# Kernel tuning notes

Measured on AMD Instinct MI355X. Metric: run time of the kernel, lower is better.

## Reference

```python
import jax, jax.numpy as jnp
import numpy as np

L, D, H, DK, S, B = 6, 1024, 16, 64, 512, 8
DFF = 4 * D
NEG = -1.0e9


def layer_norm(x, g, b, eps=1e-5):
    mu = jnp.mean(x, axis=-1, keepdims=True)
    var = jnp.var(x, axis=-1, keepdims=True)
    return (x - mu) * jax.lax.rsqrt(var + eps) * g + b


def setup_inputs() -> dict:
    key = jax.random.key(0)
    ks = jax.random.split(key, 16)
    s = 0.02
    inp = {
        "x": jax.random.normal(ks[0], (B, S, D), jnp.float32),
        "mask": jax.random.bernoulli(ks[1], 0.1, (B, S, S)),
        "relation": jax.random.normal(ks[2], (B, S, S), jnp.float32) * 0.1,
        # per-layer params (stacked over L)
        "Wq": jax.random.normal(ks[3], (L, D, H * DK), jnp.float32) * s,
        "Wk": jax.random.normal(ks[4], (L, D, H * DK), jnp.float32) * s,
        "Wv": jax.random.normal(ks[5], (L, D, H * DK), jnp.float32) * s,
        "Wo": jax.random.normal(ks[6], (L, H * DK, D), jnp.float32) * s,
        "bo": jnp.zeros((L, D), jnp.float32),
        "ln_g": jnp.ones((L, D), jnp.float32),   # EncoderLayer.norm (shared pre-attn / pre-FFN)
        "ln_b": jnp.zeros((L, D), jnp.float32),
        "ln2_g": jnp.ones((L, D), jnp.float32),  # AttSubLayerv2.norm
        "ln2_b": jnp.zeros((L, D), jnp.float32),
        "W1": jax.random.normal(ks[7], (L, D, DFF), jnp.float32) * s,
        "b1": jnp.zeros((L, DFF), jnp.float32),
        "W2": jax.random.normal(ks[8], (L, DFF, D), jnp.float32) * s,
        "b2": jnp.zeros((L, D), jnp.float32),
        "lnf_g": jnp.ones((D,), jnp.float32),    # Encoder.norm
        "lnf_b": jnp.zeros((D,), jnp.float32),
    }
    return inp


def reference(x, mask, relation, Wq, Wk, Wv, Wo, bo, ln_g, ln_b, ln2_g, ln2_b,
              W1, b1, W2, b2, lnf_g, lnf_b):
    # dropout layers run in eval mode (identity)
    scale = 1.0 / jnp.sqrt(jnp.asarray(DK, x.dtype))
    h = x
    attns = []
    for l in range(L):
        q_in = layer_norm(h, ln_g[l], ln_b[l])
        # AttSubLayerv2
        def proj(W):
            return jnp.einsum('bsd,de->bse', q_in, W).reshape(h.shape[0], -1, H, DK).transpose(0, 2, 1, 3)
        Q, K, V = proj(Wq[l]), proj(Wk[l]), proj(Wv[l])  # [B,H,S,DK]
        qk = jnp.einsum('bhqd,bhkd->bhqk', Q, K)
        scores = jnp.einsum('bhqk,bkn->bhqn', qk, relation) * scale
        scores = jnp.where(mask[:, None], NEG, scores)
        p = jax.nn.softmax(scores, axis=-1)  # [B,H,S,S]
        att = jnp.einsum('bhqk,bhkd->bhqd', p, V).transpose(0, 2, 1, 3).reshape(h.shape[0], -1, H * DK)
        att = att @ Wo[l] + bo[l]
        att_out = layer_norm(att + q_in, ln2_g[l], ln2_b[l])
        h = h + att_out
        # FFN (pre-norm with shared EncoderLayer norm)
        f = layer_norm(h, ln_g[l], ln_b[l])
        h = h + (jax.nn.relu(f @ W1[l] + b1[l]) @ W2[l] + b2[l])
        attns.append(p)
    out = layer_norm(h, lnf_g, lnf_b)
    return out, jnp.stack(attns)
```

## Files before the change

### kernel.cpp

```cpp
#include <hip/hip_runtime.h>
#include <hip/hip_bf16.h>
#include <stdint.h>

#define LL 6
#define DD 1024
#define HH 16
#define DKK 64
#define SS 512
#define BB 8
#define DFF_ 4096
#define BS (BB*SS)
#define NEGV -1.0e9f

typedef __attribute__((ext_vector_type(8))) short short8;
typedef __attribute__((ext_vector_type(4))) float f32x4;
typedef __attribute__((ext_vector_type(4))) unsigned short ushort4v;

static __device__ __forceinline__ float bf2f(unsigned short u){
  union { unsigned int i; float f; } v; v.i = ((unsigned int)u)<<16; return v.f;
}
static __device__ __forceinline__ unsigned short f2bf(float f){
  union { float f; unsigned int i; } v; v.f=f;
  unsigned int r = v.i + 0x7fff + ((v.i>>16)&1);
  return (unsigned short)(r>>16);
}

static __device__ __forceinline__ void gload16(const void* g, void* l){
  __builtin_amdgcn_global_load_lds((const __attribute__((address_space(1))) unsigned int*)g,
                                   (__attribute__((address_space(3))) unsigned int*)l, 16, 0, 0);
}

struct TrDesc { const float* in; unsigned short* out; long is1,is2,os1,os2; int ldin,ldout,zd,gx,gy; };
struct TrPack { TrDesc d[7]; int cum[8]; };

__global__ void __launch_bounds__(256) tr_multi_k(TrPack P)
{
  __shared__ float t[32][33];
  int bid=blockIdx.x, di=0;
  #pragma unroll
  for(int k=1;k<7;k++) if(bid>=P.cum[k]) di=k;
  TrDesc dd=P.d[di];
  int local=bid-P.cum[di];
  int bx=local%dd.gx; int rest=local/dd.gx;
  int by=rest%dd.gy; int z=rest/dd.gy;
  int z1=z/dd.zd, z2=z%dd.zd;
  const float* ip=dd.in+z1*dd.is1+z2*dd.is2;
  unsigned short* op=dd.out+z1*dd.os1+z2*dd.os2;
  int r0=by*32, c0=bx*32;
  int tx=threadIdx.x, ty=threadIdx.y;
  #pragma unroll
  for(int i=0;i<4;i++)
    t[ty+i*8][tx] = ip[(long)(r0+ty+i*8)*dd.ldin + c0+tx];
  __syncthreads();
  #pragma unroll
  for(int i=0;i<4;i++)
    op[(long)(c0+ty+i*8)*dd.ldout + r0+tx] = f2bf(t[tx][ty+i*8]);
}

__global__ void __launch_bounds__(256) maskpack_k(const int* __restrict__ mask, unsigned* __restrict__ mb)
{
  int idx = blockIdx.x*256 + threadIdx.x;
  int row = idx>>4, w = idx&15;
  const int* mp = mask + (long)row*SS + w*32;
  unsigned v=0;
  #pragma unroll
  for(int i=0;i<32;i++) v |= (mp[i]!=0) ? (1u<<i) : 0u;
  mb[idx]=v;
}

__global__ void __launch_bounds__(256) ln_k(const float* __restrict__ src,
    const float* __restrict__ gw, const float* __restrict__ bw,
    float* __restrict__ outf, unsigned short* __restrict__ outb,
    const float* __restrict__ resid)
{
  long row=blockIdx.x;
  float4 v=((const float4*)(src+row*DD))[threadIdx.x];
  float s=v.x+v.y+v.z+v.w;
  float s2=v.x*v.x+v.y*v.y+v.z*v.z+v.w*v.w;
  #pragma unroll
  for(int o=32;o;o>>=1){ s+=__shfl_xor(s,o); s2+=__shfl_xor(s2,o); }
  __shared__ float red[8];
  int wid=threadIdx.x>>6, lane=threadIdx.x&63;
  if(lane==0){ red[wid]=s; red[4+wid]=s2; }
  __syncthreads();
  s=red[0]+red[1]+red[2]+red[3];
  s2=red[4]+red[5]+red[6]+red[7];
  float mu=s*(1.f/DD);
  float rstd=rsqrtf(s2*(1.f/DD)-mu*mu+1e-5f);
  int c=threadIdx.x*4;
  float4 g4=*(const float4*)(gw+c), b4=*(const float4*)(bw+c);
  float4 o;
  o.x=(v.x-mu)*rstd*g4.x+b4.x;
  o.y=(v.y-mu)*rstd*g4.y+b4.y;
  o.z=(v.z-mu)*rstd*g4.z+b4.z;
  o.w=(v.w-mu)*rstd*g4.w+b4.w;
  if(resid){
    float4 r4=((const float4*)(resid+row*DD))[threadIdx.x];
    o.x+=r4.x; o.y+=r4.y; o.z+=r4.z; o.w+=r4.w;
  }
  if(outf) ((float4*)(outf+row*DD))[threadIdx.x]=o;
  if(outb){
    uint2 pk;
    pk.x=(unsigned)f2bf(o.x)|((unsigned)f2bf(o.y)<<16);
    pk.y=(unsigned)f2bf(o.z)|((unsigned)f2bf(o.w)<<16);
    ((uint2*)(outb+row*DD))[threadIdx.x]=pk;
  }
}

__global__ void __launch_bounds__(256) ln2_k(const float* __restrict__ src,
    const float* __restrict__ resid,
    const float* __restrict__ g2, const float* __restrict__ b2,
    const float* __restrict__ g1, const float* __restrict__ b1,
    float* __restrict__ outf, unsigned short* __restrict__ outb)
{
  long row=blockIdx.x;
  int wid=threadIdx.x>>6, lane=threadIdx.x&63, c=threadIdx.x*4;
  __shared__ float red[8];
  float4 v=((const float4*)(src+row*DD))[threadIdx.x];
  float s=v.x+v.y+v.z+v.w;
  float s2=v.x*v.x+v.y*v.y+v.z*v.z+v.w*v.w;
  #pragma unroll
  for(int o=32;o;o>>=1){ s+=__shfl_xor(s,o); s2+=__shfl_xor(s2,o); }
  if(lane==0){ red[wid]=s; red[4+wid]=s2; }
  __syncthreads();
  s=red[0]+red[1]+red[2]+red[3];
  s2=red[4]+red[5]+red[6]+red[7];
  float mu=s*(1.f/DD);
  float rstd=rsqrtf(s2*(1.f/DD)-mu*mu+1e-5f);
  float4 g4=*(const float4*)(g2+c), b4=*(const float4*)(b2+c);
  float4 r4=((const float4*)(resid+row*DD))[threadIdx.x];
  float4 o;
  o.x=(v.x-mu)*rstd*g4.x+b4.x+r4.x;
  o.y=(v.y-mu)*rstd*g4.y+b4.y+r4.y;
  o.z=(v.z-mu)*rstd*g4.z+b4.z+r4.z;
  o.w=(v.w-mu)*rstd*g4.w+b4.w+r4.w;
  ((float4*)(outf+row*DD))[threadIdx.x]=o;
  s=o.x+o.y+o.z+o.w;
  s2=o.x*o.x+o.y*o.y+o.z*o.z+o.w*o.w;
  #pragma unroll
  for(int of=32;of;of>>=1){ s+=__shfl_xor(s,of); s2+=__shfl_xor(s2,of); }
  __syncthreads();
  if(lane==0){ red[wid]=s; red[4+wid]=s2; }
  __syncthreads();
  s=red[0]+red[1]+red[2]+red[3];
  s2=red[4]+red[5]+red[6]+red[7];
  mu=s*(1.f/DD);
  rstd=rsqrtf(s2*(1.f/DD)-mu*mu+1e-5f);
  g4=*(const float4*)(g1+c); b4=*(const float4*)(b1+c);
  uint2 pk;
  pk.x=(unsigned)f2bf((o.x-mu)*rstd*g4.x+b4.x)|((unsigned)f2bf((o.y-mu)*rstd*g4.y+b4.y)<<16);
  pk.y=(unsigned)f2bf((o.z-mu)*rstd*g4.z+b4.z)|((unsigned)f2bf((o.w-mu)*rstd*g4.w+b4.w)<<16);
  ((uint2*)(outb+row*DD))[threadIdx.x]=pk;
}

struct GemmP {
  const unsigned short* A; long sA1; int ldA;
  const unsigned short* B; long sB1; int ldB;
  float* outF; unsigned short* outB; long sO1; int ldO;
  const float* bias;
  const float* residF; int ldR;
  const unsigned short* residB;
  unsigned short *kt, *vt;
  int K, relu, mb;
};

template<int MODE,int BM,int BN,int WM,int WN>
__global__ void __launch_bounds__(WM*WN*64,2) gemm2p_k(GemmP p)
{
  constexpr int NW=WM*WN, BK=64;
  constexpr int WRT=BM/WM, WCT=BN/WN;
  constexpr int FM=WRT/16, FN=WCT/16;
  constexpr int RG=NW*8;
  constexpr int BUFE=(BM+BN)*BK;
  __shared__ __align__(16) unsigned short smem[2*BUFE];
  const int tid=threadIdx.x, lane=tid&63, wid=tid>>6;
  const int wr=wid/WN, wc=wid%WN;
  const int lr=lane&15, lk=(lane>>4)*8;
  const int nwg=gridDim.x, bid=blockIdx.x;
  const int nb=(bid&7)*(nwg>>3)+(bid>>3);
  const int m0=(nb%p.mb)*BM, n0=(nb/p.mb)*BN;
  const int z=blockIdx.y;
  const unsigned short* Ap=p.A+(long)z*p.sA1;
  const unsigned short* Bp=p.B+(long)z*p.sB1;
  const int NT=p.K/BK;

  const int sr8=lane>>3;
  const int scol=((lane&7)^sr8)<<3;

  #define STG(T,BI) { \
    const long kb_=(long)(T)*BK; \
    unsigned short* As_=smem+(BI)*BUFE; \
    unsigned short* Bs_=As_+BM*BK; \
    _Pragma("unroll") \
    for(int L=0;L<BM/RG;L++){ int r_=L*RG+wid*8+sr8; \
      gload16(Ap+(long)(m0+r_)*p.ldA+kb_+scol, As_+(L*RG+wid*8)*BK); } \
    _Pragma("unroll") \
    for(int L=0;L<BN/RG;L++){ int r_=L*RG+wid*8+sr8; \
      gload16(Bp+(long)(n0+r_)*p.ldB+kb_+scol, Bs_+(L*RG+wid*8)*BK); } }

  f32x4 acc[FM][FN];
  #pragma unroll
  for(int m=0;m<FM;m++)
    #pragma unroll
    for(int n=0;n<FN;n++) acc[m][n]=(f32x4){0.f,0.f,0.f,0.f};

  STG(0,0);
  asm volatile("s_waitcnt vmcnt(0)" ::: "memory");
  __builtin_amdgcn_sched_barrier(0);
  __builtin_amdgcn_s_barrier();
  __builtin_amdgcn_sched_barrier(0);

  const int xr=(lr&7)<<3;
  int cur=0;
  for(int t=0;t<NT;t++){
    if(t+1<NT) STG(t+1,cur^1);
    const unsigned short* As=smem+cur*BUFE;
    const unsigned short* Bs=As+BM*BK;
    #pragma unroll
    for(int kk=0;kk<2;kk++){
      short8 a[FM], b[FN];
      #pragma unroll
      for(int m=0;m<FM;m++) a[m]=*(const short8*)(As+(wr*WRT+m*16+lr)*BK+((kk*32+lk)^xr));
      #pragma unroll
      for(int n=0;n<FN;n++) b[n]=*(const short8*)(Bs+(wc*WCT+n*16+lr)*BK+((kk*32+lk)^xr));
      __builtin_amdgcn_s_setprio(1);
      #pragma unroll
      for(int m=0;m<FM;m++)
        #pragma unroll
        for(int n=0;n<FN;n++)
          acc[m][n]=__builtin_amdgcn_mfma_f32_16x16x32_bf16(a[m],b[n],acc[m][n],0,0,0);
      __builtin_amdgcn_s_setprio(0);
    }
    asm volatile("s_waitcnt vmcnt(0)" ::: "memory");
    __builtin_amdgcn_sched_barrier(0);
    __builtin_amdgcn_s_barrier();
    __builtin_amdgcn_sched_barrier(0);
    cur^=1;
  }
  #undef STG

  const int rl=(lane>>4)*4;
  if(MODE==1){
    int sec = n0>>10;
    #pragma unroll
    for(int m=0;m<FM;m++){
      int gr0 = m0 + wr*WRT + m*16 + rl;
      int b = gr0>>9, s0 = gr0&511;
      #pragma unroll
      for(int n=0;n<FN;n++){
        int gc = n0 + wc*WCT + n*16 + lr;
        if(sec==0){
          #pragma unroll
          for(int r=0;r<4;r++)
            p.outB[(long)(gr0+r)*1024 + gc] = f2bf(acc[m][n][r]);
        } else {
          unsigned short* dst = sec==1 ? p.kt : p.vt;
          int hh=(gc>>6)&15, d=gc&63;
          ushort4v pk;
          pk.x=f2bf(acc[m][n][0]); pk.y=f2bf(acc[m][n][1]);
          pk.z=f2bf(acc[m][n][2]); pk.w=f2bf(acc[m][n][3]);
          *(ushort4v*)(dst + (((long)b*HH+hh)*DKK+d)*SS + s0) = pk;
        }
      }
    }
  } else {
    #pragma unroll
    for(int m=0;m<FM;m++){
      int gr0 = m0 + wr*WRT + m*16 + rl;
      #pragma unroll
      for(int n=0;n<FN;n++){
        int gc = n0 + wc*WCT + n*16 + lr;
        float bv = p.bias ? p.bias[gc] : 0.f;
        #pragma unroll
        for(int r=0;r<4;r++){
          long ro=(long)(gr0+r);
          float val=acc[m][n][r]+bv;
          if(p.relu) val=fmaxf(val,0.f);
          if(p.residF) val += p.residF[ro*(long)p.ldR+gc];
          if(p.residB) val += bf2f(p.residB[ro*(long)p.ldR+gc]);
          long oo = (long)z*p.sO1 + ro*(long)p.ldO+gc;
          if(p.outF) p.outF[oo]=val;
          if(p.outB) p.outB[oo]=f2bf(val);
        }
      }
    }
  }
}

template<int MODE,int BM,int BN,int WM,int WN>
static inline void launch_gemm2p(GemmP& p,int M,int N,int Z,hipStream_t s){
  p.mb=M/BM;
  gemm2p_k<MODE,BM,BN,WM,WN><<<dim3((M/BM)*(N/BN),Z),dim3(WM*WN*64),0,s>>>(p);
}

__global__ void __launch_bounds__(512) att_k(const unsigned short* __restrict__ Qb,
    const unsigned short* __restrict__ KRT, float* __restrict__ pout,
    const unsigned* __restrict__ maskb, const unsigned short* __restrict__ Vt,
    unsigned short* __restrict__ attb)
{
  constexpr int BM=128, BK=32, NT=512;
  constexpr int FM=4, FN=8;
  __shared__ __align__(16) char smem[49152];
  unsigned short* As = (unsigned short*)smem;
  unsigned short* Bs = (unsigned short*)(smem+8192);
  unsigned short* Ps = (unsigned short*)smem;
  unsigned short* Vs = (unsigned short*)(smem+32768);
  __shared__ float redmx[BM][4];
  __shared__ float redsm[BM][4];
  int bh = blockIdx.y; int b = bh>>4, h = bh&15;
  const unsigned short* Ap = Qb + (long)b*SS*1024 + h*64;
  const unsigned short* Bp = KRT + (long)b*SS*1024 + h*64;
  int m0 = blockIdx.x*BM;
  int tid=threadIdx.x, lane=tid&63, wid=tid>>6;
  int wr=wid>>2, wc=wid&3;
  f32x4 acc[FM][FN];
  #pragma unroll
  for(int i=0;i<FM;i++)
    #pragma unroll
    for(int j=0;j<FN;j++) acc[i][j]=(f32x4){0.f,0.f,0.f,0.f};
  const int lr=lane&15, lk=(lane>>4)*8;
  for(int k0=0;k0<DKK;k0+=BK){
    { int v=tid;
      gload16(Ap + (long)(m0+(v>>2))*1024 + k0 + (v&3)*8, As + (wid*64)*8); }
    #pragma unroll
    for(int r=0;r<4;r++){
      int v=r*NT+tid;
      gload16(Bp + (long)(v>>2)*1024 + k0 + (v&3)*8, Bs + (r*NT+wid*64)*8);
    }
    __syncthreads();
    short8 af[FM], bfr[FN];
    #pragma unroll
    for(int i=0;i<FM;i++) af[i]=*(const short8*)(As + (wr*64+i*16+lr)*BK + lk);
    #pragma unroll
    for(int j=0;j<FN;j++) bfr[j]=*(const short8*)(Bs + (wc*128+j*16+lr)*BK + lk);
    #pragma unroll
    for(int i=0;i<FM;i++)
      #pragma unroll
      for(int j=0;j<FN;j++)
        acc[i][j]=__builtin_amdgcn_mfma_f32_16x16x32_bf16(af[i],bfr[j],acc[i][j],0,0,0);
    __syncthreads();
  }
  const int rl=(lane>>4)*4;
  #pragma unroll
  for(int i=0;i<FM;i++){
    #pragma unroll
    for(int r=0;r<4;r++){
      int row=wr*64+i*16+rl+r;
      uint4 mw = *((const uint4*)(maskb + ((long)(b*SS+m0+row))*16 + wc*4));
      float m_=-3.4e38f;
      #pragma unroll
      for(int j=0;j<FN;j++){
        unsigned word = (j>>1)==0? mw.x : (j>>1)==1? mw.y : (j>>1)==2? mw.z : mw.w;
        float v = ((word>>(((j&1)<<4)+lr))&1) ? NEGV : acc[i][j][r]*0.125f;
        acc[i][j][r]=v; m_=fmaxf(m_,v);
      }
      #pragma unroll
      for(int o=1;o<16;o<<=1) m_=fmaxf(m_,__shfl_xor(m_,o));
      if(lr==0) redmx[row][wc]=m_;
    }
  }
  __syncthreads();
  #pragma unroll
  for(int i=0;i<FM;i++){
    #pragma unroll
    for(int r=0;r<4;r++){
      int row=wr*64+i*16+rl+r;
      float m_=fmaxf(fmaxf(redmx[row][0],redmx[row][1]),fmaxf(redmx[row][2],redmx[row][3]));
      float s_=0.f;
      #pragma unroll
      for(int j=0;j<FN;j++){
        float e=__expf(acc[i][j][r]-m_);
        acc[i][j][r]=e; s_+=e;
      }
      #pragma unroll
      for(int o=1;o<16;o<<=1) s_+=__shfl_xor(s_,o);
      if(lr==0) redsm[row][wc]=s_;
    }
  }
  __syncthreads();
  #pragma unroll
  for(int i=0;i<FM;i++){
    #pragma unroll
    for(int r=0;r<4;r++){
      int row=wr*64+i*16+rl+r;
      float inv=1.f/(redsm[row][0]+redsm[row][1]+redsm[row][2]+redsm[row][3]);
      long obase=((long)bh*SS + m0+row)*(long)SS;
      #pragma unroll
      for(int j=0;j<FN;j++){
        int col=wc*128+j*16+lr;
        float pv=acc[i][j][r]*inv;
        acc[i][j][r]=pv;
        pout[obase+col]=pv;
      }
    }
  }
  __syncthreads();
  f32x4 attacc[4];
  #pragma unroll
  for(int j=0;j<4;j++) attacc[j]=(f32x4){0.f,0.f,0.f,0.f};
  for(int kc=0;kc<4;kc++){
    #pragma unroll
    for(int r2=0;r2<2;r2++){
      int v=r2*512+tid;
      int d=v>>4, m=v&15;
      int u=m^(d&7);
      gload16(Vt + ((long)bh*64 + d)*512 + kc*128 + u*8, Vs + (r2*512 + wid*64)*8);
    }
    if(wc==kc){
      #pragma unroll
      for(int i=0;i<FM;i++){
        #pragma unroll
        for(int r=0;r<4;r++){
          int row=wr*64+i*16+rl+r;
          #pragma unroll
          for(int j=0;j<FN;j++){
            int col=j*16+lr;
            Ps[row*128 + (col ^ ((row&7)<<3))] = f2bf(acc[i][j][r]);
          }
        }
      }
    }
    __syncthreads();
    #pragma unroll
    for(int kk=0;kk<4;kk++){
      int arow=wid*16+lr;
      short8 paf=*(const short8*)(Ps + arow*128 + ((kk*32+lk) ^ ((arow&7)<<3)));
      #pragma unroll
      for(int j=0;j<4;j++){
        int d=j*16+lr;
        short8 vbf=*(const short8*)(Vs + d*128 + ((kk*32+lk) ^ ((d&7)<<3)));
        attacc[j]=__builtin_amdgcn_mfma_f32_16x16x32_bf16(paf,vbf,attacc[j],0,0,0);
      }
    }
    __syncthreads();
  }
  #pragma unroll
  for(int j=0;j<4;j++){
    #pragma unroll
    for(int r=0;r<4;r++){
      int row = m0 + wid*16 + rl + r;
      attb[((long)b*SS + row)*DD + h*64 + j*16 + lr] = f2bf(attacc[j][r]);
    }
  }
}

extern "C" void kernel_launch(void* const* d_in, const int* in_sizes, int n_in,
                              void* d_out, int out_size, void* d_ws, size_t ws_size,
                              hipStream_t stream)
{
  const float* x    =(const float*)d_in[0];
  const int*   mask =(const int*)d_in[1];
  const float* rel  =(const float*)d_in[2];
  const float* Wq   =(const float*)d_in[3];
  const float* Wk   =(const float*)d_in[4];
  const float* Wv   =(const float*)d_in[5];
  const float* Wo   =(const float*)d_in[6];
  const float* bo   =(const float*)d_in[7];
  const float* ln_g =(const float*)d_in[8];
  const float* ln_b =(const float*)d_in[9];
  const float* ln2_g=(const float*)d_in[10];
  const float* ln2_b=(const float*)d_in[11];
  const float* W1   =(const float*)d_in[12];
  const float* b1   =(const float*)d_in[13];
  const float* W2   =(const float*)d_in[14];
  const float* b2   =(const float*)d_in[15];
  const float* lnf_g=(const float*)d_in[16];
  const float* lnf_b=(const float*)d_in[17];
  float* out=(float*)d_out;

  char* w=(char*)d_ws;
  auto alloc=[&](long bytes)->void*{ void* p=(void*)w; w += (bytes+255)&~255L; return p; };
  unsigned short* WTqkv=(unsigned short*)alloc((long)LL*3072*1024*2);
  unsigned short* WoT  =(unsigned short*)alloc((long)LL*1024*1024*2);
  unsigned short* W1T  =(unsigned short*)alloc((long)LL*DFF_*DD*2);
  unsigned short* W2T  =(unsigned short*)alloc((long)LL*DD*DFF_*2);
  unsigned short* relT =(unsigned short*)alloc((long)BB*SS*SS*2);
  unsigned short* qin_b=(unsigned short*)alloc((long)BS*DD*2);
  unsigned short* Qb   =(unsigned short*)alloc((long)BS*1024*2);
  unsigned short* Vt   =(unsigned short*)alloc((long)BB*HH*DKK*SS*2);
  unsigned short* Kt   =(unsigned short*)alloc((long)BB*HH*DKK*SS*2);
  unsigned short* KRT  =(unsigned short*)alloc((long)BB*SS*1024*2);
  unsigned short* attb =(unsigned short*)alloc((long)BS*DD*2);
  float*          attres=(float*)alloc((long)BS*DD*4);
  unsigned short* gbuf =(unsigned short*)alloc((long)BS*DFF_*2);
  float*          hbuf =(float*)alloc((long)BS*DD*4);
  unsigned*       maskb=(unsigned*)alloc((long)BS*16*4);
  (void)ws_size; (void)in_sizes; (void)n_in; (void)out_size;

  TrPack tp;
  auto set=[&](int i, const float* in, unsigned short* o, int ldin, int ldout,
               long is1, long os1, int zd, long is2, long os2, int gx, int gy){
    tp.d[i]={in,o,is1,is2,os1,os2,ldin,ldout,zd,gx,gy};
  };
  set(0, Wq, WTqkv,           1024,1024,(long)1024*1024,(long)3072*1024,1,0,0, 32,32);
  set(1, Wk, WTqkv+1024*1024, 1024,1024,(long)1024*1024,(long)3072*1024,1,0,0, 32,32);
  set(2, Wv, WTqkv+2048*1024, 1024,1024,(long)1024*1024,(long)3072*1024,1,0,0, 32,32);
  set(3, Wo, WoT,             1024,1024,(long)1024*1024,(long)1024*1024,1,0,0, 32,32);
  set(4, W1, W1T, 4096,1024,(long)1024*4096,(long)1024*4096,1,0,0, 128,32);
  set(5, W2, W2T, 1024,4096,(long)4096*1024,(long)4096*1024,1,0,0, 32,128);
  set(6, rel, relT, 512,512,(long)512*512,(long)512*512,1,0,0, 16,16);
  int nb[7]={32*32*LL,32*32*LL,32*32*LL,32*32*LL,128*32*LL,32*128*LL,16*16*BB};
  tp.cum[0]=0;
  for(int i=0;i<7;i++) tp.cum[i+1]=tp.cum[i]+nb[i];
  tr_multi_k<<<dim3(tp.cum[7]),dim3(32,8),0,stream>>>(tp);
  maskpack_k<<<dim3(BS*16/256),dim3(256),0,stream>>>(mask, maskb);

  const float* hin = x;
  for(int l=0;l<LL;l++){
    ln_k<<<dim3(BS),dim3(256),0,stream>>>(hin, ln_g+l*DD, ln_b+l*DD, (float*)nullptr, qin_b, (const float*)nullptr);
    { GemmP p{}; p.A=qin_b; p.ldA=DD; p.B=WTqkv+(long)l*3072*1024; p.ldB=DD;
      p.outB=Qb; p.kt=Kt; p.vt=Vt; p.K=DD;
      launch_gemm2p<1,256,256,2,4>(p, BS, 3072, 1, stream); }
    { GemmP p{}; p.A=relT; p.sA1=(long)SS*SS; p.ldA=SS;
      p.B=Kt; p.sB1=(long)HH*DKK*SS; p.ldB=SS;
      p.outB=KRT; p.sO1=(long)SS*1024; p.ldO=1024; p.K=SS;
      launch_gemm2p<0,128,128,2,2>(p, SS, 1024, BB, stream); }
    float* attn_l = out + (long)BS*DD + (long)l*BB*HH*SS*SS;
    att_k<<<dim3(SS/128, BB*HH),dim3(512),0,stream>>>(Qb, KRT, attn_l, maskb, Vt, attb);
    { GemmP p{}; p.A=attb; p.ldA=DD; p.B=WoT+(long)l*1024*1024; p.ldB=DD;
      p.outF=attres; p.ldO=DD; p.bias=bo+l*DD;
      p.residB=qin_b; p.ldR=DD; p.K=DD;
      launch_gemm2p<0,128,128,2,2>(p, BS, DD, 1, stream); }
    ln2_k<<<dim3(BS),dim3(256),0,stream>>>(attres, hin, ln2_g+l*DD, ln2_b+l*DD,
        ln_g+l*DD, ln_b+l*DD, hbuf, qin_b);
    { GemmP p{}; p.A=qin_b; p.ldA=DD; p.B=W1T+(long)l*DFF_*DD; p.ldB=DD;
      p.outB=gbuf; p.ldO=DFF_; p.bias=b1+l*DFF_; p.relu=1; p.K=DD;
      launch_gemm2p<0,256,256,2,4>(p, BS, DFF_, 1, stream); }
    { GemmP p{}; p.A=gbuf; p.ldA=DFF_; p.B=W2T+(long)l*DD*DFF_; p.ldB=DFF_;
      p.outF=hbuf; p.ldO=DD; p.bias=b2+l*DD;
      p.residF=hbuf; p.ldR=DD; p.K=DFF_;
      launch_gemm2p<0,128,128,2,2>(p, BS, DD, 1, stream); }
    hin=hbuf;
  }
  ln_k<<<dim3(BS),dim3(256),0,stream>>>(hbuf, lnf_g, lnf_b, out, (unsigned short*)nullptr, (const float*)nullptr);
}
```

Measured before the change: 2.205 ms.

## Replace templated GEMM with fixed 128x128 8-wave kernel and 4-stage smem pipeline

Replaces the parameterised double-buffered GEMM with a single 128x128 tile kernel using 8 waves (2x4), a four-buffer LDS ring that prefetches two K-steps ahead, and one barrier per two K-steps. The XCD-aware block swizzle is dropped in favour of a plain 3D grid. All GEMMs, including the large QKV and FFN1 ones that used 256x256 tiles, now use this kernel. The intent is better latency hiding and fewer barriers, at the cost of smaller tiles on the big GEMMs (less reuse per load), 128 KB of LDS per block, which may limit occupancy, and loss of L2 locality from the swizzle.

```diff
diff --git a/kernel.cpp b/kernel.cpp
--- a/kernel.cpp
+++ b/kernel.cpp
@@ -161,94 +161,94 @@
   const float* residF; int ldR;
   const unsigned short* residB;
   unsigned short *kt, *vt;
-  int K, relu, mb;
+  int K, relu;
 };
 
-template<int MODE,int BM,int BN,int WM,int WN>
-__global__ void __launch_bounds__(WM*WN*64,2) gemm2p_k(GemmP p)
-{
-  constexpr int NW=WM*WN, BK=64;
-  constexpr int WRT=BM/WM, WCT=BN/WN;
-  constexpr int FM=WRT/16, FN=WCT/16;
-  constexpr int RG=NW*8;
+template<int MODE>
+__global__ void __launch_bounds__(512,2) gemm8_k(GemmP p)
+{
+  constexpr int BM=128, BN=128, BK=64;
   constexpr int BUFE=(BM+BN)*BK;
-  __shared__ __align__(16) unsigned short smem[2*BUFE];
+  constexpr int FN=2;
+  constexpr int WNT=32;
+  __shared__ __align__(16) unsigned short smem[4*BUFE];
   const int tid=threadIdx.x, lane=tid&63, wid=tid>>6;
-  const int wr=wid/WN, wc=wid%WN;
+  const int wr=wid>>2, wc=wid&3;
   const int lr=lane&15, lk=(lane>>4)*8;
-  const int nwg=gridDim.x, bid=blockIdx.x;
-  const int nb=(bid&7)*(nwg>>3)+(bid>>3);
-  const int m0=(nb%p.mb)*BM, n0=(nb/p.mb)*BN;
-  const int z=blockIdx.y;
+  const int m0=blockIdx.y*BM, n0=blockIdx.x*BN;
+  const int z=blockIdx.z;
   const unsigned short* Ap=p.A+(long)z*p.sA1;
   const unsigned short* Bp=p.B+(long)z*p.sB1;
   const int NT=p.K/BK;
 
-  const int sr8=lane>>3;
-  const int scol=((lane&7)^sr8)<<3;
-
-  #define STG(T,BI) { \
+  const int sr8 = lane>>3;
+  const int scol = ((lane&7) ^ sr8) << 3;
+
+  #define STAGE8(T,BI) { \
     const long kb_=(long)(T)*BK; \
     unsigned short* As_=smem+(BI)*BUFE; \
     unsigned short* Bs_=As_+BM*BK; \
     _Pragma("unroll") \
-    for(int L=0;L<BM/RG;L++){ int r_=L*RG+wid*8+sr8; \
-      gload16(Ap+(long)(m0+r_)*p.ldA+kb_+scol, As_+(L*RG+wid*8)*BK); } \
+    for(int L=0;L<2;L++){ \
+      int r_=L*64+wid*8+sr8; \
+      gload16(Ap+(long)(m0+r_)*p.ldA+kb_+scol, As_+L*4096+wid*512); \
+    } \
     _Pragma("unroll") \
-    for(int L=0;L<BN/RG;L++){ int r_=L*RG+wid*8+sr8; \
-      gload16(Bp+(long)(n0+r_)*p.ldB+kb_+scol, Bs_+(L*RG+wid*8)*BK); } }
-
-  f32x4 acc[FM][FN];
-  #pragma unroll
-  for(int m=0;m<FM;m++)
+    for(int L=0;L<2;L++){ \
+      int r_=L*64+wid*8+sr8; \
+      gload16(Bp+(long)(n0+r_)*p.ldB+kb_+scol, Bs_+L*4096+wid*512); \
+    } }
+
+  f32x4 acc[4][FN];
+  #pragma unroll
+  for(int m=0;m<4;m++)
     #pragma unroll
     for(int n=0;n<FN;n++) acc[m][n]=(f32x4){0.f,0.f,0.f,0.f};
 
-  STG(0,0);
-  asm volatile("s_waitcnt vmcnt(0)" ::: "memory");
-  __builtin_amdgcn_sched_barrier(0);
-  __builtin_amdgcn_s_barrier();
-  __builtin_amdgcn_sched_barrier(0);
-
-  const int xr=(lr&7)<<3;
-  int cur=0;
-  for(int t=0;t<NT;t++){
-    if(t+1<NT) STG(t+1,cur^1);
-    const unsigned short* As=smem+cur*BUFE;
-    const unsigned short* Bs=As+BM*BK;
-    #pragma unroll
-    for(int kk=0;kk<2;kk++){
-      short8 a[FM], b[FN];
-      #pragma unroll
-      for(int m=0;m<FM;m++) a[m]=*(const short8*)(As+(wr*WRT+m*16+lr)*BK+((kk*32+lk)^xr));
-      #pragma unroll
-      for(int n=0;n<FN;n++) b[n]=*(const short8*)(Bs+(wc*WCT+n*16+lr)*BK+((kk*32+lk)^xr));
-      __builtin_amdgcn_s_setprio(1);
-      #pragma unroll
-      for(int m=0;m<FM;m++)
+  STAGE8(0,0);
+  STAGE8(1,1);
+  __syncthreads();
+
+  const int xr = (lr&7)<<3;
+  for(int t=0;t<NT;t+=2){
+    if(t+2<NT) STAGE8(t+2,(t+2)&3);
+    if(t+3<NT) STAGE8(t+3,(t+3)&3);
+    #pragma unroll
+    for(int u=0;u<2;u++){
+      const unsigned short* As=smem+((t+u)&3)*BUFE;
+      const unsigned short* Bs=As+BM*BK;
+      #pragma unroll
+      for(int kk=0;kk<2;kk++){
+        short8 a[4], b[FN];
+        #pragma unroll
+        for(int m=0;m<4;m++)
+          a[m]=*(const short8*)(As + (wr*64+m*16+lr)*BK + ((kk*32+lk)^xr));
         #pragma unroll
         for(int n=0;n<FN;n++)
-          acc[m][n]=__builtin_amdgcn_mfma_f32_16x16x32_bf16(a[m],b[n],acc[m][n],0,0,0);
-      __builtin_amdgcn_s_setprio(0);
-    }
-    asm volatile("s_waitcnt vmcnt(0)" ::: "memory");
-    __builtin_amdgcn_sched_barrier(0);
-    __builtin_amdgcn_s_barrier();
-    __builtin_amdgcn_sched_barrier(0);
-    cur^=1;
-  }
-  #undef STG
+          b[n]=*(const short8*)(Bs + (wc*WNT+n*16+lr)*BK + ((kk*32+lk)^xr));
+        __builtin_amdgcn_s_setprio(1);
+        #pragma unroll
+        for(int m=0;m<4;m++)
+          #pragma unroll
+          for(int n=0;n<FN;n++)
+            acc[m][n]=__builtin_amdgcn_mfma_f32_16x16x32_bf16(a[m],b[n],acc[m][n],0,0,0);
+        __builtin_amdgcn_s_setprio(0);
+      }
+    }
+    __syncthreads();
+  }
+  #undef STAGE8
 
   const int rl=(lane>>4)*4;
   if(MODE==1){
     int sec = n0>>10;
     #pragma unroll
-    for(int m=0;m<FM;m++){
-      int gr0 = m0 + wr*WRT + m*16 + rl;
+    for(int m=0;m<4;m++){
+      int gr0 = m0 + wr*64 + m*16 + rl;
       int b = gr0>>9, s0 = gr0&511;
       #pragma unroll
       for(int n=0;n<FN;n++){
-        int gc = n0 + wc*WCT + n*16 + lr;
+        int gc = n0 + wc*WNT + n*16 + lr;
         if(sec==0){
           #pragma unroll
           for(int r=0;r<4;r++)
@@ -265,11 +265,11 @@
     }
   } else {
     #pragma unroll
-    for(int m=0;m<FM;m++){
-      int gr0 = m0 + wr*WRT + m*16 + rl;
+    for(int m=0;m<4;m++){
+      int gr0 = m0 + wr*64 + m*16 + rl;
       #pragma unroll
       for(int n=0;n<FN;n++){
-        int gc = n0 + wc*WCT + n*16 + lr;
+        int gc = n0 + wc*WNT + n*16 + lr;
         float bv = p.bias ? p.bias[gc] : 0.f;
         #pragma unroll
         for(int r=0;r<4;r++){
@@ -287,10 +287,9 @@
   }
 }
 
-template<int MODE,int BM,int BN,int WM,int WN>
-static inline void launch_gemm2p(GemmP& p,int M,int N,int Z,hipStream_t s){
-  p.mb=M/BM;
-  gemm2p_k<MODE,BM,BN,WM,WN><<<dim3((M/BM)*(N/BN),Z),dim3(WM*WN*64),0,s>>>(p);
+template<int MODE>
+static inline void launch_gemm8(GemmP& p,int M,int N,int Z,hipStream_t s){
+  gemm8_k<MODE><<<dim3(N/128,M/128,Z),dim3(512),0,s>>>(p);
 }
 
 __global__ void __launch_bounds__(512) att_k(const unsigned short* __restrict__ Qb,
@@ -510,26 +509,26 @@
     ln_k<<<dim3(BS),dim3(256),0,stream>>>(hin, ln_g+l*DD, ln_b+l*DD, (float*)nullptr, qin_b, (const float*)nullptr);
     { GemmP p{}; p.A=qin_b; p.ldA=DD; p.B=WTqkv+(long)l*3072*1024; p.ldB=DD;
       p.outB=Qb; p.kt=Kt; p.vt=Vt; p.K=DD;
-      launch_gemm2p<1,256,256,2,4>(p, BS, 3072, 1, stream); }
+      launch_gemm8<1>(p, BS, 3072, 1, stream); }
     { GemmP p{}; p.A=relT; p.sA1=(long)SS*SS; p.ldA=SS;
       p.B=Kt; p.sB1=(long)HH*DKK*SS; p.ldB=SS;
       p.outB=KRT; p.sO1=(long)SS*1024; p.ldO=1024; p.K=SS;
-      launch_gemm2p<0,128,128,2,2>(p, SS, 1024, BB, stream); }
+      launch_gemm8<0>(p, SS, 1024, BB, stream); }
     float* attn_l = out + (long)BS*DD + (long)l*BB*HH*SS*SS;
     att_k<<<dim3(SS/128, BB*HH),dim3(512),0,stream>>>(Qb, KRT, attn_l, maskb, Vt, attb);
     { GemmP p{}; p.A=attb; p.ldA=DD; p.B=WoT+(long)l*1024*1024; p.ldB=DD;
       p.outF=attres; p.ldO=DD; p.bias=bo+l*DD;
       p.residB=qin_b; p.ldR=DD; p.K=DD;
-      launch_gemm2p<0,128,128,2,2>(p, BS, DD, 1, stream); }
+      launch_gemm8<0>(p, BS, DD, 1, stream); }
     ln2_k<<<dim3(BS),dim3(256),0,stream>>>(attres, hin, ln2_g+l*DD, ln2_b+l*DD,
         ln_g+l*DD, ln_b+l*DD, hbuf, qin_b);
     { GemmP p{}; p.A=qin_b; p.ldA=DD; p.B=W1T+(long)l*DFF_*DD; p.ldB=DD;
       p.outB=gbuf; p.ldO=DFF_; p.bias=b1+l*DFF_; p.relu=1; p.K=DD;
-      launch_gemm2p<0,256,256,2,4>(p, BS, DFF_, 1, stream); }
+      launch_gemm8<0>(p, BS, DFF_, 1, stream); }
     { GemmP p{}; p.A=gbuf; p.ldA=DFF_; p.B=W2T+(long)l*DD*DFF_; p.ldB=DFF_;
       p.outF=hbuf; p.ldO=DD; p.bias=b2+l*DD;
       p.residF=hbuf; p.ldR=DD; p.K=DFF_;
-      launch_gemm2p<0,128,128,2,2>(p, BS, DD, 1, stream); }
+      launch_gemm8<0>(p, BS, DD, 1, stream); }
     hin=hbuf;
   }
   ln_k<<<dim3(BS),dim3(256),0,stream>>>(hbuf, lnf_g, lnf_b, out, (unsigned short*)nullptr, (const float*)nullptr);
```

Result: faster. 2.076 ms (-5.9%).
